# Kernel optimization log

Hardware: AMD Instinct MI355X
Metric: run time of the kernel (lower is better)

The kernel has to match this reference:

```python
import jax, jax.numpy as jnp
import numpy as np

INPUT_SIZE = 64
RESERVOIR_SIZE = 2048
SPECTRAL_RADIUS = 0.9
SPARSITY = 0.1
WARMUP = 100
LEAKING_RATE = 0.01
T = 8192


def _make_weights(seed=0):
    rng = np.random.default_rng(seed)
    Win = (rng.random((RESERVOIR_SIZE, INPUT_SIZE)) - 0.5).astype(np.float32)
    Wh = (rng.random((RESERVOIR_SIZE, RESERVOIR_SIZE)) - 0.5).astype(np.float32)
    # scale to spectral radius, then apply sparsity mask (same order as the torch module)
    eig = np.linalg.eigvals(Wh.astype(np.float64))
    Wh = Wh * np.float32(SPECTRAL_RADIUS / np.max(np.abs(eig)))
    mask = (rng.random((RESERVOIR_SIZE, RESERVOIR_SIZE)) < SPARSITY).astype(np.float32)
    Wh = Wh * mask
    return jnp.asarray(Win), jnp.asarray(Wh)


def setup_inputs() -> dict:
    key = jax.random.key(0)
    x = jax.random.normal(key, (T, INPUT_SIZE), dtype=jnp.float32)
    Win, Wh = _make_weights()
    return {"x": x, "Win": Win, "Wh": Wh}


def reference(x, Win, Wh):
    lr = jnp.float32(LEAKING_RATE)

    def step(h, xt):
        h_new = jnp.tanh(Win @ xt + Wh @ h)
        h = (1.0 - lr) * h + lr * h_new
        return h, jnp.concatenate([h, xt])  # extended state [R + I]

    h0 = jnp.zeros((RESERVOIR_SIZE,), dtype=x.dtype)
    _, H_all = jax.lax.scan(step, h0, x)  # [T, R + I]
    return H_all[WARMUP:]                 # [T - warmup, R + I]
```

## Files before the change

### kernel.cpp

```cpp
#include <hip/hip_runtime.h>
#include <hip/hip_fp16.h>
#include <math.h>


#define NWG        128
#define ROWS_PER_WG 16
#define T_STEPS    8192
#define WARMUP     100
#define RSIZE      2048
#define ISIZE      64
#define OUTCOLS    2112
#define SEGPAD     528

__global__ __launch_bounds__(256) void init_ws_kernel(unsigned* buf0, unsigned* buf1) {
    int t = blockIdx.x * blockDim.x + threadIdx.x;
    if (t < RSIZE) {
        buf0[t] = 0u;
        buf1[t] = 0xFFFF0000u;
    }
}

__global__ __launch_bounds__(256) void xcopy_kernel(const float* __restrict__ x,
                                                    float* __restrict__ out) {
    int t = blockIdx.x * blockDim.x + threadIdx.x;
    if (t >= (T_STEPS - WARMUP) * ISIZE) return;
    int rowo = t >> 6;
    int j    = t & 63;
    out[(size_t)rowo * OUTCOLS + RSIZE + j] = x[(size_t)(rowo + WARMUP) * ISIZE + j];
}

static __device__ __forceinline__ float h16_to_f32(unsigned short u) {
    __half_raw hr; hr.x = u;
    return __half2float(__half(hr));
}
static __device__ __forceinline__ unsigned short f32_to_h16(float f) {
    __half_raw hr = __half_raw(__float2half_rn(f));
    return hr.x;
}

#define W_FOREACH(F) \
    F(0)  F(1)  F(2)  F(3)  F(4)  F(5)  F(6)  F(7)  \
    F(8)  F(9)  F(10) F(11) F(12) F(13) F(14) F(15) \
    F(16) F(17) F(18) F(19) F(20) F(21) F(22) F(23) \
    F(24) F(25) F(26) F(27) F(28) F(29) F(30) F(31)

__global__ __launch_bounds__(256, 1) void esn_scan_kernel(
    const float* __restrict__ x,
    const float* __restrict__ Win,
    const float* __restrict__ Wh,
    float* __restrict__ out,
    unsigned* buf0,
    unsigned* buf1)
{
    __shared__ float hs[4 * SEGPAD];
    __shared__ float part[64];

    const int tid = threadIdx.x;
    const int wg  = blockIdx.x;
    const int w   = tid >> 6;
    const int l   = tid & 63;
    const int r4  = l >> 2;
    const int c4  = l & 3;
    const int row = wg * ROWS_PER_WG + r4;
    const int seg = w * 512;

    const float4* whp4 = (const float4*)(Wh + (size_t)row * RSIZE + seg + c4 * 128);
#define DECL_W(J) \
    float w##J##x, w##J##y, w##J##z, w##J##w; \
    { float4 t = whp4[J]; \
      w##J##x = t.x; w##J##y = t.y; w##J##z = t.z; w##J##w = t.w; } \
    asm volatile("" : "+v"(w##J##x), "+v"(w##J##y), "+v"(w##J##z), "+v"(w##J##w));
    W_FOREACH(DECL_W)
#undef DECL_W
    float wix, wiy, wiz, wiw;
    { float4 t = *(const float4*)(Win + (size_t)row * ISIZE + w * 16 + c4 * 4);
      wix = t.x; wiy = t.y; wiz = t.z; wiw = t.w; }
    asm volatile("" : "+v"(wix), "+v"(wiy), "+v"(wiz), "+v"(wiw));

    float hcur = 0.0f;

    for (int k = 1; k <= T_STEPS; ++k) {
        const float4 xv = *(const float4*)(x + (size_t)(k - 1) * ISIZE + w * 16 + c4 * 4);

        const unsigned* bp = ((k - 1) & 1) ? buf1 : buf0;
        const unsigned expect = (unsigned)(k - 1) << 16;
        unsigned wv[8];
        unsigned mask = 0xFFu;
        while (mask) {
#pragma unroll
            for (int s = 0; s < 8; ++s) {
                if (mask & (1u << s)) {
                    wv[s] = __hip_atomic_load(bp + w * 512 + s * 64 + l,
                                              __ATOMIC_RELAXED, __HIP_MEMORY_SCOPE_AGENT);
                }
            }
#pragma unroll
            for (int s = 0; s < 8; ++s) {
                if ((mask & (1u << s)) && (wv[s] & 0xFFFF0000u) == expect) {
                    mask &= ~(1u << s);
                }
            }
        }

        float* hw = hs + w * SEGPAD;
#pragma unroll
        for (int s = 0; s < 8; ++s) {
            int col  = s * 64 + l;
            int addr = col + ((col >> 7) << 2);
            hw[addr] = h16_to_f32((unsigned short)(wv[s] & 0xFFFFu));
        }

        float p = wix * xv.x + wiy * xv.y + wiz * xv.z + wiw * xv.w;
        const float* hb = hw + c4 * 132;
#define FMA_W(J) { const float4 hv = *(const float4*)(hb + 4 * J); \
                   p += w##J##x * hv.x + w##J##y * hv.y \
                      + w##J##z * hv.z + w##J##w * hv.w; }
        W_FOREACH(FMA_W)
#undef FMA_W

        p += __shfl_xor(p, 1);
        p += __shfl_xor(p, 2);
        if (c4 == 0) part[r4 * 4 + w] = p;

        __syncthreads();

        if (tid < 16) {
            const float4 ps = *(const float4*)(part + tid * 4);
            float y = ps.x + ps.y + ps.z + ps.w;
            float ax = fabsf(y);
            float e  = __expf(2.0f * ax);
            float t  = 1.0f - 2.0f / (e + 1.0f);
            t = copysignf(t, y);
            hcur = 0.99f * hcur + 0.01f * t;

            unsigned* bc = (k & 1) ? buf1 : buf0;
            unsigned word = ((unsigned)k << 16) | (unsigned)f32_to_h16(hcur);
            __hip_atomic_store(bc + wg * ROWS_PER_WG + tid, word,
                               __ATOMIC_RELAXED, __HIP_MEMORY_SCOPE_AGENT);
            if (k >= WARMUP + 1) {
                out[(size_t)(k - (WARMUP + 1)) * OUTCOLS + wg * ROWS_PER_WG + tid] = hcur;
            }
        }
    }
}

extern "C" void kernel_launch(void* const* d_in, const int* in_sizes, int n_in,
                              void* d_out, int out_size, void* d_ws, size_t ws_size,
                              hipStream_t stream) {
    const float* x   = (const float*)d_in[0];
    const float* Win = (const float*)d_in[1];
    const float* Wh  = (const float*)d_in[2];
    float* out = (float*)d_out;

    char* ws = (char*)d_ws;
    unsigned* buf0 = (unsigned*)ws;
    unsigned* buf1 = (unsigned*)(ws + RSIZE * 4);

    init_ws_kernel<<<8, 256, 0, stream>>>(buf0, buf1);

    {
        int n = (T_STEPS - WARMUP) * ISIZE;
        xcopy_kernel<<<(n + 255) / 256, 256, 0, stream>>>(x, out);
    }

    esn_scan_kernel<<<NWG, 256, 0, stream>>>(x, Win, Wh, out, buf0, buf1);
}
```

Baseline: 19.38 ms.

## Replicate step-exchange buffers across workgroups and poll with 64-bit loads

Each workgroup now writes its new hidden-state words into up to eight replicated exchange buffers, and readers are spread across the replicas by workgroup index. This is meant to reduce contention on the shared polling addresses in the per-step grid-wide handoff. Polling also switches from eight 32-bit atomic loads per lane to four 64-bit loads, each checking two tagged halves at once, which halves the number of poll instructions. The cost is extra stores per step from the 16 writer threads and more workspace use, with the replica count chosen from the workspace size.

```diff
diff --git a/kernel.cpp b/kernel.cpp
--- a/kernel.cpp
+++ b/kernel.cpp
@@ -11,12 +11,17 @@
 #define ISIZE      64
 #define OUTCOLS    2112
 #define SEGPAD     528
+#define MAXREP     8
+#define REP_STRIDE_W 16384
 
-__global__ __launch_bounds__(256) void init_ws_kernel(unsigned* buf0, unsigned* buf1) {
+__global__ __launch_bounds__(256) void init_ws_kernel(unsigned* rep0, int nrep) {
     int t = blockIdx.x * blockDim.x + threadIdx.x;
-    if (t < RSIZE) {
-        buf0[t] = 0u;
-        buf1[t] = 0xFFFF0000u;
+    if (t < nrep * RSIZE) {
+        int rep = t >> 11;
+        int idx = t & (RSIZE - 1);
+        unsigned* b = rep0 + rep * REP_STRIDE_W;
+        b[idx]         = 0u;
+        b[RSIZE + idx] = 0xFFFF0000u;
     }
 }
 
@@ -49,8 +54,8 @@
     const float* __restrict__ Win,
     const float* __restrict__ Wh,
     float* __restrict__ out,
-    unsigned* buf0,
-    unsigned* buf1)
+    unsigned* rep0,
+    int nrep, int repmask)
 {
     __shared__ float hs[4 * SEGPAD];
     __shared__ float part[64];
@@ -63,6 +68,8 @@
     const int c4  = l & 3;
     const int row = wg * ROWS_PER_WG + r4;
     const int seg = w * 512;
+
+    const unsigned* myrep = rep0 + (wg & repmask) * REP_STRIDE_W;
 
     const float4* whp4 = (const float4*)(Wh + (size_t)row * RSIZE + seg + c4 * 128);
 #define DECL_W(J) \
@@ -82,32 +89,37 @@
     for (int k = 1; k <= T_STEPS; ++k) {
         const float4 xv = *(const float4*)(x + (size_t)(k - 1) * ISIZE + w * 16 + c4 * 4);
 
-        const unsigned* bp = ((k - 1) & 1) ? buf1 : buf0;
-        const unsigned expect = (unsigned)(k - 1) << 16;
-        unsigned wv[8];
-        unsigned mask = 0xFFu;
-        while (mask) {
+        const unsigned* bp = myrep + (((k - 1) & 1) ? RSIZE : 0) + seg;
+        const unsigned long long exp64 =
+            ((unsigned long long)(unsigned)(k - 1) << 16) * 0x100000001ull;
+        unsigned long long q[4];
+        unsigned m = 0xFu;
+        while (m) {
 #pragma unroll
-            for (int s = 0; s < 8; ++s) {
-                if (mask & (1u << s)) {
-                    wv[s] = __hip_atomic_load(bp + w * 512 + s * 64 + l,
-                                              __ATOMIC_RELAXED, __HIP_MEMORY_SCOPE_AGENT);
+            for (int s = 0; s < 4; ++s) {
+                if (m & (1u << s)) {
+                    q[s] = __hip_atomic_load(
+                        (const unsigned long long*)(bp + s * 128 + 2 * l),
+                        __ATOMIC_RELAXED, __HIP_MEMORY_SCOPE_AGENT);
                 }
             }
 #pragma unroll
-            for (int s = 0; s < 8; ++s) {
-                if ((mask & (1u << s)) && (wv[s] & 0xFFFF0000u) == expect) {
-                    mask &= ~(1u << s);
+            for (int s = 0; s < 4; ++s) {
+                if ((m & (1u << s)) &&
+                    (q[s] & 0xFFFF0000FFFF0000ull) == exp64) {
+                    m &= ~(1u << s);
                 }
             }
         }
 
         float* hw = hs + w * SEGPAD;
 #pragma unroll
-        for (int s = 0; s < 8; ++s) {
-            int col  = s * 64 + l;
-            int addr = col + ((col >> 7) << 2);
-            hw[addr] = h16_to_f32((unsigned short)(wv[s] & 0xFFFFu));
+        for (int s = 0; s < 4; ++s) {
+            float2* d = (float2*)(hw + 132 * s + 2 * l);
+            float2 v;
+            v.x = h16_to_f32((unsigned short)(q[s] & 0xFFFFu));
+            v.y = h16_to_f32((unsigned short)((q[s] >> 32) & 0xFFFFu));
+            *d = v;
         }
 
         float p = wix * xv.x + wiy * xv.y + wiz * xv.z + wiw * xv.w;
@@ -133,10 +145,15 @@
             t = copysignf(t, y);
             hcur = 0.99f * hcur + 0.01f * t;
 
-            unsigned* bc = (k & 1) ? buf1 : buf0;
             unsigned word = ((unsigned)k << 16) | (unsigned)f32_to_h16(hcur);
-            __hip_atomic_store(bc + wg * ROWS_PER_WG + tid, word,
-                               __ATOMIC_RELAXED, __HIP_MEMORY_SCOPE_AGENT);
+            const int slot = ((k & 1) ? RSIZE : 0) + wg * ROWS_PER_WG + tid;
+#pragma unroll
+            for (int rr = 0; rr < MAXREP; ++rr) {
+                if (rr < nrep) {
+                    __hip_atomic_store(rep0 + rr * REP_STRIDE_W + slot, word,
+                                       __ATOMIC_RELAXED, __HIP_MEMORY_SCOPE_AGENT);
+                }
+            }
             if (k >= WARMUP + 1) {
                 out[(size_t)(k - (WARMUP + 1)) * OUTCOLS + wg * ROWS_PER_WG + tid] = hcur;
             }
@@ -152,16 +169,21 @@
     const float* Wh  = (const float*)d_in[2];
     float* out = (float*)d_out;
 
-    char* ws = (char*)d_ws;
-    unsigned* buf0 = (unsigned*)ws;
-    unsigned* buf1 = (unsigned*)(ws + RSIZE * 4);
+    unsigned* rep0 = (unsigned*)d_ws;
 
-    init_ws_kernel<<<8, 256, 0, stream>>>(buf0, buf1);
+    int nrep = MAXREP;
+    while (nrep > 1 && (size_t)nrep * (REP_STRIDE_W * 4) > ws_size) nrep >>= 1;
+    int repmask = nrep - 1;
+
+    {
+        int n = nrep * RSIZE;
+        init_ws_kernel<<<(n + 255) / 256, 256, 0, stream>>>(rep0, nrep);
+    }
 
     {
         int n = (T_STEPS - WARMUP) * ISIZE;
         xcopy_kernel<<<(n + 255) / 256, 256, 0, stream>>>(x, out);
     }
 
-    esn_scan_kernel<<<NWG, 256, 0, stream>>>(x, Win, Wh, out, buf0, buf1);
+    esn_scan_kernel<<<NWG, 256, 0, stream>>>(x, Win, Wh, out, rep0, nrep, repmask);
 }
```

Result: faster. 18.36 ms (-5.3%).
